# Performance work log

Measured on AMD Instinct MI355X. Metric: run time of the kernel, lower is better.

Reference implementation:

```python
import jax, jax.numpy as jnp
import numpy as np

EMBED_SIZE = 1024
HEADS = 16
HEAD_DIM = EMBED_SIZE // HEADS


def setup_inputs() -> dict:
    key = jax.random.key(0)
    k1, k2, k3, k4 = jax.random.split(key, 4)
    N, L = 4, 2048
    return {
        "values": jax.random.normal(k1, (N, L, EMBED_SIZE), dtype=jnp.float32),
        "keys": jax.random.normal(k2, (N, L, EMBED_SIZE), dtype=jnp.float32),
        "query": jax.random.normal(k3, (N, L, EMBED_SIZE), dtype=jnp.float32),
        "w_out": jax.random.normal(k4, (EMBED_SIZE, EMBED_SIZE), dtype=jnp.float32) * (1.0 / np.sqrt(EMBED_SIZE)),
        "b_out": jnp.zeros((EMBED_SIZE,), dtype=jnp.float32),
    }


def reference(values, keys, query, w_out, b_out):
    N, q_len, _ = query.shape
    v_len = values.shape[1]
    k_len = keys.shape[1]
    # split heads: (N, L, H, D). NOTE: source never applies the per-head
    # q/k/v Linear layers in forward, so raw inputs are used directly.
    v = values.reshape(N, v_len, HEADS, HEAD_DIM)
    k = keys.reshape(N, k_len, HEADS, HEAD_DIM)
    q = query.reshape(N, q_len, HEADS, HEAD_DIM)
    # energy: (N, H, Q, K); scale by sqrt(embed_size) as in the source
    energy = jnp.einsum('nqhd,nkhd->nhqk', q, k)
    attn = jax.nn.softmax(energy / jnp.sqrt(jnp.float32(EMBED_SIZE)), axis=3)
    out = jnp.einsum('nhql,nlhd->nqhd', attn, v).reshape(N, q_len, EMBED_SIZE)
    # fc_out: x @ W.T + b (torch Linear convention)
    return out @ w_out.T + b_out
```

## Files before the change

### kernel.cpp

```cpp
#include <hip/hip_runtime.h>
#include <hip/hip_bf16.h>

#define NB 4
#define LSEQ 2048
#define NH 16
#define HD 64
#define EMB 1024

typedef __attribute__((ext_vector_type(8))) short bf16x8;
typedef __attribute__((ext_vector_type(4))) float f32x4;
typedef __attribute__((ext_vector_type(16))) float f32x16;
typedef __attribute__((ext_vector_type(2))) unsigned int uint2v;

__device__ __forceinline__ unsigned short f2bf(float x) {
    union { float f; unsigned u; } v; v.f = x;
    unsigned r = v.u + 0x7fff + ((v.u >> 16) & 1);
    return (unsigned short)(r >> 16);
}

__device__ __forceinline__ float exp2_fast(float x) {
#if __has_builtin(__builtin_amdgcn_exp2f)
    return __builtin_amdgcn_exp2f(x);
#else
    float r; asm("v_exp_f32 %0, %1\n\ts_nop 1" : "=v"(r) : "v"(x)); return r;
#endif
}

__device__ __forceinline__ unsigned pack_bf2(float lo, float hi) {
    union { __hip_bfloat162 h2; unsigned u; } cv;
    cv.h2 = __float22bfloat162_rn(make_float2(lo, hi));
    return cv.u;
}

__device__ __forceinline__ void plswap(unsigned &a, unsigned &b) {
#if __has_builtin(__builtin_amdgcn_permlane32_swap)
    uint2v r = __builtin_amdgcn_permlane32_swap(a, b, false, false);
    a = r[0]; b = r[1];
#else
    asm volatile("s_nop 0\n\tv_permlane32_swap_b32 %0, %1\n\ts_nop 0"
                 : "+v"(a), "+v"(b));
#endif
}

__device__ __forceinline__ void async16(void* lds, const void* g) {
    __builtin_amdgcn_global_load_lds(
        (const __attribute__((address_space(1))) unsigned int*)g,
        (__attribute__((address_space(3))) unsigned int*)lds, 16, 0, 0);
}

__global__ void wconv_kernel(const float* __restrict__ Wf, unsigned short* __restrict__ Wb) {
    int i = (blockIdx.x * 256 + threadIdx.x) * 4;
    float4 v = *(const float4*)(Wf + i);
    ushort4 o = { f2bf(v.x), f2bf(v.y), f2bf(v.z), f2bf(v.w) };
    *(ushort4*)(Wb + i) = o;
}

__global__ void prep_all(const float* __restrict__ Wf, unsigned short* __restrict__ Wb,
                         const float* __restrict__ Kf, unsigned short* __restrict__ Kb,
                         const float* __restrict__ Vf, unsigned short* __restrict__ Vt)
{
    __shared__ float T[64][65];
    const int tid = threadIdx.x;
    const int b = blockIdx.x;

    if (b < 1024) {
        int i = (b * 256 + tid) * 4;
        float4 v = *(const float4*)(Wf + i);
        ushort4 o = { f2bf(v.x), f2bf(v.y), f2bf(v.z), f2bf(v.w) };
        *(ushort4*)(Wb + i) = o;
        return;
    }
    if (b < 5120) {
        int idx = (b - 1024) * 256 + tid;
        int c   = idx & 7;
        int key = (idx >> 3) & 2047;
        int h   = (idx >> 14) & 15;
        int n   = idx >> 18;
        const float* src = Kf + (size_t)(n * LSEQ + key) * EMB + h * HD + c * 8;
        float4 a = *(const float4*)src;
        float4 bb = *(const float4*)(src + 4);
        unsigned short* dst = Kb + (((size_t)(n * NH + h) * LSEQ + key) << 6)
                                 + ((c ^ (key & 7)) << 3);
        ushort4 o0 = { f2bf(a.x), f2bf(a.y), f2bf(a.z), f2bf(a.w) };
        ushort4 o1 = { f2bf(bb.x), f2bf(bb.y), f2bf(bb.z), f2bf(bb.w) };
        *(ushort4*)dst = o0;
        *(ushort4*)(dst + 4) = o1;
        return;
    }
    {
        const int vb = b - 5120;
        const int kt = vb & 31, h = (vb >> 5) & 15, n = vb >> 9;
        const float* src = Vf + (size_t)(n * LSEQ + kt * 64) * EMB + h * HD;
        unsigned short* dst = Vt + ((size_t)vb << 12);

        for (int i = tid; i < 1024; i += 256) {
            const int key = i >> 4;
            const int c4  = (i & 15) * 4;
            const float4 v = *(const float4*)(src + (size_t)key * EMB + c4);
            T[key][c4 + 0] = v.x; T[key][c4 + 1] = v.y;
            T[key][c4 + 2] = v.z; T[key][c4 + 3] = v.w;
        }
        __syncthreads();
        for (int i = tid; i < 512; i += 256) {
            const int d = i >> 3, c = i & 7;
            ushort4 o0 = { f2bf(T[c * 8 + 0][d]), f2bf(T[c * 8 + 1][d]),
                           f2bf(T[c * 8 + 2][d]), f2bf(T[c * 8 + 3][d]) };
            ushort4 o1 = { f2bf(T[c * 8 + 4][d]), f2bf(T[c * 8 + 5][d]),
                           f2bf(T[c * 8 + 6][d]), f2bf(T[c * 8 + 7][d]) };
            unsigned short* p = dst + (d << 6) + ((c ^ (d & 7)) << 3);
            *(ushort4*)p = o0;
            *(ushort4*)(p + 4) = o1;
        }
    }
}

__global__ __launch_bounds__(256, 2)
void attn13_kernel(const float* __restrict__ Qq, const unsigned short* __restrict__ Kb,
                   const unsigned short* __restrict__ Vt, unsigned short* __restrict__ X)
{
    __shared__ unsigned short Kl[3][4096];
    __shared__ unsigned short Vl[3][4096];

    const int tid  = threadIdx.x;
    const int lane = tid & 63;
    const int w    = tid >> 6;
    const int l31  = lane & 31;
    const int hl   = lane >> 5;
    const int swz7 = lane & 7;
    const int l    = ((blockIdx.x & 7) << 6) + (blockIdx.x >> 3);
    const int nh   = l >> 3;
    const int qtile = l & 7;
    const int n = nh >> 4, h = nh & 15;
    const int qrow0 = qtile * 256 + w * 64;

    bf16x8 ones;
    #pragma unroll
    for (int e = 0; e < 8; ++e) ones[e] = (short)0x3F80;

    const float qscale = 0.03125f * 1.44269504f;
    bf16x8 qf[2][4];
    #pragma unroll
    for (int g = 0; g < 2; ++g) {
        const float* qp = Qq + (size_t)(n * LSEQ + qrow0 + g * 32 + l31) * EMB + h * HD + hl * 8;
        #pragma unroll
        for (int dk = 0; dk < 4; ++dk) {
            bf16x8 t;
            #pragma unroll
            for (int e = 0; e < 8; ++e) t[e] = (short)f2bf(qp[dk * 16 + e] * qscale);
            qf[g][dk] = t;
        }
    }

    f32x16 oaccT[2][2];
    f32x16 lacc[2];
    #pragma unroll
    for (int g = 0; g < 2; ++g) {
        #pragma unroll
        for (int e = 0; e < 16; ++e) lacc[g][e] = 0.f;
        #pragma unroll
        for (int db = 0; db < 2; ++db)
            #pragma unroll
            for (int e = 0; e < 16; ++e) oaccT[g][db][e] = 0.f;
    }

    const unsigned short* kg0 = Kb + ((size_t)nh << 17);
    const unsigned short* vg0 = Vt + ((size_t)nh << 17);
    const int t8 = tid << 3;

#define ATTN_STAGE(buf, kt)                                                  \
    {                                                                        \
        const unsigned short* kg = kg0 + ((kt) << 12) + t8;                  \
        const unsigned short* vg = vg0 + ((kt) << 12) + t8;                  \
        async16(&Kl[buf][t8],        kg);                                    \
        async16(&Kl[buf][t8 + 2048], kg + 2048);                             \
        async16(&Vl[buf][t8],        vg);                                    \
        async16(&Vl[buf][t8 + 2048], vg + 2048);                             \
    }

    ATTN_STAGE(0, 0)
    ATTN_STAGE(1, 1)
    asm volatile("s_waitcnt vmcnt(4)" ::: "memory");
    __builtin_amdgcn_s_barrier();

    int cur = 0;
    for (int kt = 0; kt < LSEQ / 64; ++kt) {
        if (kt + 2 < LSEQ / 64) {
            const int pre = cur >= 1 ? cur - 1 : cur + 2;
            ATTN_STAGE(pre, kt + 2)
        }

        #pragma unroll
        for (int kb = 0; kb < 2; ++kb) {
            f32x16 sk[2];
            #pragma unroll
            for (int g = 0; g < 2; ++g)
                #pragma unroll
                for (int e = 0; e < 16; ++e) sk[g][e] = 0.f;
            #pragma unroll
            for (int dk = 0; dk < 4; ++dk) {
                bf16x8 ka = *(const bf16x8*)&Kl[cur][((kb * 32 + l31) << 6) + (((2 * dk + hl) ^ swz7) << 3)];
                #pragma unroll
                for (int g = 0; g < 2; ++g)
                    sk[g] = __builtin_amdgcn_mfma_f32_32x32x16_bf16(ka, qf[g][dk], sk[g], 0, 0, 0);
            }

            unsigned wgt[2][4][2];
            #pragma unroll
            for (int g = 0; g < 2; ++g) {
                float p[16];
                #pragma unroll
                for (int e = 0; e < 16; ++e) p[e] = exp2_fast(sk[g][e]);
                #pragma unroll
                for (int gg = 0; gg < 4; ++gg) {
                    wgt[g][gg][0] = pack_bf2(p[4 * gg + 0], p[4 * gg + 1]);
                    wgt[g][gg][1] = pack_bf2(p[4 * gg + 2], p[4 * gg + 3]);
                }
                plswap(wgt[g][0][0], wgt[g][1][0]); plswap(wgt[g][0][1], wgt[g][1][1]);
                plswap(wgt[g][2][0], wgt[g][3][0]); plswap(wgt[g][2][1], wgt[g][3][1]);
            }

            #pragma unroll
            for (int ks = 0; ks < 2; ++ks) {
                union { unsigned u[4]; bf16x8 v; } pu[2];
                #pragma unroll
                for (int g = 0; g < 2; ++g) {
                    pu[g].u[0] = wgt[g][2 * ks + 0][0];
                    pu[g].u[1] = wgt[g][2 * ks + 0][1];
                    pu[g].u[2] = wgt[g][2 * ks + 1][0];
                    pu[g].u[3] = wgt[g][2 * ks + 1][1];
                    lacc[g] = __builtin_amdgcn_mfma_f32_32x32x16_bf16(ones, pu[g].v, lacc[g], 0, 0, 0);
                }
                #pragma unroll
                for (int db = 0; db < 2; ++db) {
                    bf16x8 va = *(const bf16x8*)&Vl[cur][((db * 32 + l31) << 6) + (((4 * kb + 2 * ks + hl) ^ swz7) << 3)];
                    #pragma unroll
                    for (int g = 0; g < 2; ++g)
                        oaccT[g][db] = __builtin_amdgcn_mfma_f32_32x32x16_bf16(va, pu[g].v, oaccT[g][db], 0, 0, 0);
                }
            }
        }

        if (kt + 2 < LSEQ / 64) {
            asm volatile("s_waitcnt vmcnt(4)" ::: "memory");
        } else {
            asm volatile("s_waitcnt vmcnt(0)" ::: "memory");
        }
        __builtin_amdgcn_s_barrier();
        cur = cur < 2 ? cur + 1 : 0;
    }

    #pragma unroll
    for (int g = 0; g < 2; ++g) {
        const float rcp = 1.0f / lacc[g][0];
        unsigned ow0[4][2], ow1[4][2];
        #pragma unroll
        for (int gg = 0; gg < 4; ++gg) {
            ow0[gg][0] = pack_bf2(oaccT[g][0][4 * gg + 0] * rcp, oaccT[g][0][4 * gg + 1] * rcp);
            ow0[gg][1] = pack_bf2(oaccT[g][0][4 * gg + 2] * rcp, oaccT[g][0][4 * gg + 3] * rcp);
            ow1[gg][0] = pack_bf2(oaccT[g][1][4 * gg + 0] * rcp, oaccT[g][1][4 * gg + 1] * rcp);
            ow1[gg][1] = pack_bf2(oaccT[g][1][4 * gg + 2] * rcp, oaccT[g][1][4 * gg + 3] * rcp);
        }
        #pragma unroll
        for (int gg = 0; gg < 4; ++gg) {
            plswap(ow0[gg][0], ow1[gg][0]);
            plswap(ow0[gg][1], ow1[gg][1]);
        }
        unsigned short* xrow = X + (size_t)(n * LSEQ + qrow0 + g * 32 + l31) * EMB + h * HD + hl * 32;
        #pragma unroll
        for (int gg = 0; gg < 4; ++gg) {
            uint4 st = { ow0[gg][0], ow0[gg][1], ow1[gg][0], ow1[gg][1] };
            *(uint4*)(xrow + 8 * gg) = st;
        }
    }
}

#define KPAD 72
#define PPAD 72

__global__ __launch_bounds__(256, 2)
void attn_kernel(const float* __restrict__ Vv, const float* __restrict__ Kk,
                 const float* __restrict__ Qq, unsigned short* __restrict__ X)
{
    __shared__ unsigned short Klds[64 * KPAD];
    __shared__ unsigned short Vtlds[64 * KPAD];
    __shared__ unsigned short Plds[4 * 16 * PPAD];

    const int tid  = threadIdx.x;
    const int lane = tid & 63;
    const int w    = tid >> 6;
    const int l15  = lane & 15;
    const int l4   = lane >> 4;
    const int qtile = blockIdx.x;
    const int nh    = blockIdx.y;
    const int n = nh >> 4, h = nh & 15;

    bf16x8 qf[2];
    {
        const int qrow = qtile * 64 + w * 16 + l15;
        const float* qp = Qq + (size_t)(n * LSEQ + qrow) * EMB + h * HD + l4 * 8;
        for (int kk = 0; kk < 2; ++kk) {
            bf16x8 t;
            #pragma unroll
            for (int e = 0; e < 8; ++e) t[e] = (short)f2bf(qp[kk * 32 + e] * 0.03125f);
            qf[kk] = t;
        }
    }

    f32x4 oacc[4];
    #pragma unroll
    for (int f = 0; f < 4; ++f) oacc[f] = (f32x4){0.f, 0.f, 0.f, 0.f};
    float mrun[4], lrun[4];
    #pragma unroll
    for (int r = 0; r < 4; ++r) { mrun[r] = -1e30f; lrun[r] = 0.f; }

    for (int kt = 0; kt < LSEQ / 64; ++kt) {
        __syncthreads();
        for (int i = tid; i < 1024; i += 256) {
            const int row = i >> 4;
            const int c4  = (i & 15) * 4;
            const size_t gb = (size_t)(n * LSEQ + kt * 64 + row) * EMB + h * HD + c4;
            const float4 kv = *(const float4*)(Kk + gb);
            const float4 vv = *(const float4*)(Vv + gb);
            ushort4 k4 = { f2bf(kv.x), f2bf(kv.y), f2bf(kv.z), f2bf(kv.w) };
            *(ushort4*)&Klds[row * KPAD + c4] = k4;
            Vtlds[(c4 + 0) * KPAD + row] = f2bf(vv.x);
            Vtlds[(c4 + 1) * KPAD + row] = f2bf(vv.y);
            Vtlds[(c4 + 2) * KPAD + row] = f2bf(vv.z);
            Vtlds[(c4 + 3) * KPAD + row] = f2bf(vv.w);
        }
        __syncthreads();

        f32x4 s[4];
        #pragma unroll
        for (int f = 0; f < 4; ++f) {
            f32x4 acc = (f32x4){0.f, 0.f, 0.f, 0.f};
            #pragma unroll
            for (int kk = 0; kk < 2; ++kk) {
                bf16x8 kb = *(const bf16x8*)&Klds[(f * 16 + l15) * KPAD + kk * 32 + l4 * 8];
                acc = __builtin_amdgcn_mfma_f32_16x16x32_bf16(qf[kk], kb, acc, 0, 0, 0);
            }
            s[f] = acc;
        }

        float mnew[4], corr[4];
        #pragma unroll
        for (int r = 0; r < 4; ++r) {
            float m0 = fmaxf(fmaxf(s[0][r], s[1][r]), fmaxf(s[2][r], s[3][r]));
            #pragma unroll
            for (int msk = 1; msk < 16; msk <<= 1) m0 = fmaxf(m0, __shfl_xor(m0, msk));
            mnew[r] = fmaxf(mrun[r], m0);
            corr[r] = __expf(mrun[r] - mnew[r]);
        }
        float psum[4] = {0.f, 0.f, 0.f, 0.f};
        #pragma unroll
        for (int f = 0; f < 4; ++f) {
            #pragma unroll
            for (int r = 0; r < 4; ++r) {
                float p = __expf(s[f][r] - mnew[r]);
                psum[r] += p;
                Plds[(w * 16 + l4 * 4 + r) * PPAD + f * 16 + l15] = f2bf(p);
            }
        }
        #pragma unroll
        for (int r = 0; r < 4; ++r) {
            float t = psum[r];
            #pragma unroll
            for (int msk = 1; msk < 16; msk <<= 1) t += __shfl_xor(t, msk);
            lrun[r] = lrun[r] * corr[r] + t;
            mrun[r] = mnew[r];
        }
        #pragma unroll
        for (int f = 0; f < 4; ++f) {
            #pragma unroll
            for (int r = 0; r < 4; ++r) oacc[f][r] *= corr[r];
        }
        __syncthreads();

        #pragma unroll
        for (int ks = 0; ks < 2; ++ks) {
            bf16x8 pa = *(const bf16x8*)&Plds[(w * 16 + l15) * PPAD + ks * 32 + l4 * 8];
            #pragma unroll
            for (int f = 0; f < 4; ++f) {
                bf16x8 vb = *(const bf16x8*)&Vtlds[(f * 16 + l15) * KPAD + ks * 32 + l4 * 8];
                oacc[f] = __builtin_amdgcn_mfma_f32_16x16x32_bf16(pa, vb, oacc[f], 0, 0, 0);
            }
        }
    }

    #pragma unroll
    for (int f = 0; f < 4; ++f) {
        #pragma unroll
        for (int r = 0; r < 4; ++r) {
            const int qrow = qtile * 64 + w * 16 + l4 * 4 + r;
            const float o = oacc[f][r] / lrun[r];
            X[(size_t)(n * LSEQ + qrow) * EMB + h * HD + f * 16 + l15] = f2bf(o);
        }
    }
}

__global__ __launch_bounds__(256, 2)
void proj4_kernel(const unsigned short* __restrict__ X, const unsigned short* __restrict__ Wb,
                  const float* __restrict__ bias, float* __restrict__ out)
{
    __shared__ unsigned short Al[2][8192];
    __shared__ unsigned short Bl[2][8192];

    const int tid  = threadIdx.x;
    const int lane = tid & 63;
    const int w    = tid >> 6;
    const int l15  = lane & 15;
    const int l4   = lane >> 4;
    const int bid  = blockIdx.x;
    const int bm   = (bid & 7) * 8 + ((bid >> 3) & 7);
    const int bn   = bid >> 6;
    const int wr = (w >> 1) * 64;
    const int wc = (w & 1) * 64;

    f32x4 acc[4][4];
    #pragma unroll
    for (int i = 0; i < 4; ++i)
        #pragma unroll
        for (int j = 0; j < 4; ++j) acc[i][j] = (f32x4){0.f, 0.f, 0.f, 0.f};

    int srow[4], soff[4];
    #pragma unroll
    for (int j = 0; j < 4; ++j) {
        const int cid = tid + j * 256;
        srow[j] = cid >> 3;
        const int c = cid & 7;
        soff[j] = ((c ^ (srow[j] & 7)) << 3);
    }

#define PROJ_STAGE(buf, k0)                                                          \
    {                                                                                \
        _Pragma("unroll")                                                            \
        for (int j = 0; j < 4; ++j) {                                                \
            const int cid = tid + j * 256;                                           \
            async16(&Al[buf][cid << 3],                                              \
                    &X [(size_t)(bm * 128 + srow[j]) * EMB + (k0) + soff[j]]);       \
            async16(&Bl[buf][cid << 3],                                              \
                    &Wb[(size_t)(bn * 128 + srow[j]) * EMB + (k0) + soff[j]]);       \
        }                                                                            \
    }

    PROJ_STAGE(0, 0)
    asm volatile("s_waitcnt vmcnt(0)" ::: "memory");
    __syncthreads();

    int cur = 0;
    for (int k0 = 0; k0 < EMB; k0 += 64) {
        if (k0 + 64 < EMB) PROJ_STAGE(cur ^ 1, k0 + 64)

        #pragma unroll
        for (int kk = 0; kk < 2; ++kk) {
            bf16x8 af[4], bfr[4];
            #pragma unroll
            for (int i = 0; i < 4; ++i) {
                const int row = wr + i * 16 + l15;
                af[i] = *(const bf16x8*)&Al[cur][(row << 6) + (((kk * 4 + l4) ^ (row & 7)) << 3)];
            }
            #pragma unroll
            for (int j = 0; j < 4; ++j) {
                const int row = wc + j * 16 + l15;
                bfr[j] = *(const bf16x8*)&Bl[cur][(row << 6) + (((kk * 4 + l4) ^ (row & 7)) << 3)];
            }
            #pragma unroll
            for (int i = 0; i < 4; ++i)
                #pragma unroll
                for (int j = 0; j < 4; ++j)
                    acc[i][j] = __builtin_amdgcn_mfma_f32_16x16x32_bf16(af[i], bfr[j], acc[i][j], 0, 0, 0);
        }

        asm volatile("s_waitcnt vmcnt(0)" ::: "memory");
        __syncthreads();
        cur ^= 1;
    }

    #pragma unroll
    for (int i = 0; i < 4; ++i) {
        const int row = bm * 128 + wr + i * 16 + l4 * 4;
        #pragma unroll
        for (int j = 0; j < 4; ++j) {
            const int col = bn * 128 + wc + j * 16 + l15;
            const float bj = bias[col];
            #pragma unroll
            for (int r = 0; r < 4; ++r)
                out[(size_t)(row + r) * EMB + col] = acc[i][j][r] + bj;
        }
    }
}

extern "C" void kernel_launch(void* const* d_in, const int* in_sizes, int n_in,
                              void* d_out, int out_size, void* d_ws, size_t ws_size,
                              hipStream_t stream) {
    const float* Vv   = (const float*)d_in[0];
    const float* Kk   = (const float*)d_in[1];
    const float* Qq   = (const float*)d_in[2];
    const float* Wf   = (const float*)d_in[3];
    const float* bias = (const float*)d_in[4];
    float* out = (float*)d_out;

    unsigned short* X  = (unsigned short*)d_ws;
    unsigned short* Wb = (unsigned short*)((char*)d_ws + (size_t)16 * 1024 * 1024);
    const size_t need = (size_t)50 * 1024 * 1024;

    if (ws_size >= need) {
        unsigned short* Kb = (unsigned short*)((char*)d_ws + (size_t)18 * 1024 * 1024);
        unsigned short* Vt = (unsigned short*)((char*)d_ws + (size_t)34 * 1024 * 1024);
        prep_all<<<dim3(7168), 256, 0, stream>>>(Wf, Wb, Kk, Kb, Vv, Vt);
        attn13_kernel<<<dim3(512), 256, 0, stream>>>(Qq, Kb, Vt, X);
    } else {
        wconv_kernel<<<dim3(EMB * EMB / 1024), 256, 0, stream>>>(Wf, Wb);
        attn_kernel<<<dim3(LSEQ / 64, NB * NH), 256, 0, stream>>>(Vv, Kk, Qq, X);
    }

    proj4_kernel<<<dim3(512), 256, 0, stream>>>(X, Wb, bias, out);
}
```

Measured before the change: 128.0 us.

## Load K/V fragments directly from global into registers, drop LDS staging

The prep kernel now writes K and V in an MFMA-fragment-ready layout in 32-key chunks, so the attention kernel can load operand fragments straight from global memory into registers. This removes the LDS triple buffer, the async copies and the per-tile barriers, using a two-deep register double buffer for K instead. The row-sum is computed with scalar adds plus a cross-half shuffle rather than an extra MFMA against a ones vector. The cost is that global/L2 latency is now exposed per wave, with less prefetch depth, and each wave reloads K/V separately instead of sharing them through LDS.

Result: no change. 125.5 us (-1.9%).

```diff
diff --git a/kernel.cpp b/kernel.cpp
--- a/kernel.cpp
+++ b/kernel.cpp
@@ -79,8 +79,8 @@
         const float* src = Kf + (size_t)(n * LSEQ + key) * EMB + h * HD + c * 8;
         float4 a = *(const float4*)src;
         float4 bb = *(const float4*)(src + 4);
-        unsigned short* dst = Kb + (((size_t)(n * NH + h) * LSEQ + key) << 6)
-                                 + ((c ^ (key & 7)) << 3);
+        unsigned short* dst = Kb + ((size_t)((n * NH + h) * 64 + (key >> 5)) << 11)
+                                 + (((c << 5) + (key & 31)) << 3);
         ushort4 o0 = { f2bf(a.x), f2bf(a.y), f2bf(a.z), f2bf(a.w) };
         ushort4 o1 = { f2bf(bb.x), f2bf(bb.y), f2bf(bb.z), f2bf(bb.w) };
         *(ushort4*)dst = o0;
@@ -91,7 +91,7 @@
         const int vb = b - 5120;
         const int kt = vb & 31, h = (vb >> 5) & 15, n = vb >> 9;
         const float* src = Vf + (size_t)(n * LSEQ + kt * 64) * EMB + h * HD;
-        unsigned short* dst = Vt + ((size_t)vb << 12);
+        (void)n; (void)h; (void)kt;
 
         for (int i = tid; i < 1024; i += 256) {
             const int key = i >> 4;
@@ -102,41 +102,99 @@
         }
         __syncthreads();
         for (int i = tid; i < 512; i += 256) {
-            const int d = i >> 3, c = i & 7;
-            ushort4 o0 = { f2bf(T[c * 8 + 0][d]), f2bf(T[c * 8 + 1][d]),
-                           f2bf(T[c * 8 + 2][d]), f2bf(T[c * 8 + 3][d]) };
-            ushort4 o1 = { f2bf(T[c * 8 + 4][d]), f2bf(T[c * 8 + 5][d]),
-                           f2bf(T[c * 8 + 6][d]), f2bf(T[c * 8 + 7][d]) };
-            unsigned short* p = dst + (d << 6) + ((c ^ (d & 7)) << 3);
+            const int d = i >> 3, half = (i >> 2) & 1, c2 = i & 3;
+            const int k0 = half * 32 + c2 * 8;
+            ushort4 o0 = { f2bf(T[k0 + 0][d]), f2bf(T[k0 + 1][d]),
+                           f2bf(T[k0 + 2][d]), f2bf(T[k0 + 3][d]) };
+            ushort4 o1 = { f2bf(T[k0 + 4][d]), f2bf(T[k0 + 5][d]),
+                           f2bf(T[k0 + 6][d]), f2bf(T[k0 + 7][d]) };
+            unsigned short* p = Vt + ((size_t)(vb * 2 + half) << 11)
+                                   + (((c2 << 6) + d) << 3);
             *(ushort4*)p = o0;
             *(ushort4*)(p + 4) = o1;
         }
     }
 }
 
+
+__device__ __forceinline__ void attn14_body(
+    const bf16x8 (&KF)[4], const unsigned short* __restrict__ vb_,
+    const bf16x8 (&qf)[2][4], const int hl, const int l31,
+    f32x16 (&oaccT)[2][2], float (&lp)[2])
+{
+    bf16x8 vf[4];
+    #pragma unroll
+    for (int i = 0; i < 4; ++i) {
+        const int ks = i >> 1, db = i & 1;
+        vf[i] = *(const bf16x8*)(vb_ + ((((ks << 1) + hl) << 6) + (db << 5) + l31) * 8);
+    }
+
+    f32x16 sk[2];
+    #pragma unroll
+    for (int g = 0; g < 2; ++g)
+        #pragma unroll
+        for (int e = 0; e < 16; ++e) sk[g][e] = 0.f;
+    #pragma unroll
+    for (int dk = 0; dk < 4; ++dk)
+        #pragma unroll
+        for (int g = 0; g < 2; ++g)
+            sk[g] = __builtin_amdgcn_mfma_f32_32x32x16_bf16(KF[dk], qf[g][dk], sk[g], 0, 0, 0);
+
+    unsigned wgt[2][4][2];
+    #pragma unroll
+    for (int g = 0; g < 2; ++g) {
+        float p[16];
+        #pragma unroll
+        for (int e = 0; e < 16; ++e) p[e] = exp2_fast(sk[g][e]);
+        {
+            float t0 = (p[0] + p[1]) + (p[2] + p[3]);
+            float t1 = (p[4] + p[5]) + (p[6] + p[7]);
+            float t2 = (p[8] + p[9]) + (p[10] + p[11]);
+            float t3 = (p[12] + p[13]) + (p[14] + p[15]);
+            lp[g] += (t0 + t1) + (t2 + t3);
+        }
+        #pragma unroll
+        for (int gg = 0; gg < 4; ++gg) {
+            wgt[g][gg][0] = pack_bf2(p[4 * gg + 0], p[4 * gg + 1]);
+            wgt[g][gg][1] = pack_bf2(p[4 * gg + 2], p[4 * gg + 3]);
+        }
+        plswap(wgt[g][0][0], wgt[g][1][0]); plswap(wgt[g][0][1], wgt[g][1][1]);
+        plswap(wgt[g][2][0], wgt[g][3][0]); plswap(wgt[g][2][1], wgt[g][3][1]);
+    }
+
+    #pragma unroll
+    for (int ks = 0; ks < 2; ++ks) {
+        union { unsigned u[4]; bf16x8 v; } pu[2];
+        #pragma unroll
+        for (int g = 0; g < 2; ++g) {
+            pu[g].u[0] = wgt[g][2 * ks + 0][0];
+            pu[g].u[1] = wgt[g][2 * ks + 0][1];
+            pu[g].u[2] = wgt[g][2 * ks + 1][0];
+            pu[g].u[3] = wgt[g][2 * ks + 1][1];
+        }
+        #pragma unroll
+        for (int db = 0; db < 2; ++db)
+            #pragma unroll
+            for (int g = 0; g < 2; ++g)
+                oaccT[g][db] = __builtin_amdgcn_mfma_f32_32x32x16_bf16(vf[ks * 2 + db], pu[g].v, oaccT[g][db], 0, 0, 0);
+    }
+}
+
 __global__ __launch_bounds__(256, 2)
-void attn13_kernel(const float* __restrict__ Qq, const unsigned short* __restrict__ Kb,
+void attn14_kernel(const float* __restrict__ Qq, const unsigned short* __restrict__ Kb,
                    const unsigned short* __restrict__ Vt, unsigned short* __restrict__ X)
 {
-    __shared__ unsigned short Kl[3][4096];
-    __shared__ unsigned short Vl[3][4096];
-
     const int tid  = threadIdx.x;
     const int lane = tid & 63;
     const int w    = tid >> 6;
     const int l31  = lane & 31;
     const int hl   = lane >> 5;
-    const int swz7 = lane & 7;
     const int l    = ((blockIdx.x & 7) << 6) + (blockIdx.x >> 3);
     const int nh   = l >> 3;
     const int qtile = l & 7;
     const int n = nh >> 4, h = nh & 15;
     const int qrow0 = qtile * 256 + w * 64;
 
-    bf16x8 ones;
-    #pragma unroll
-    for (int e = 0; e < 8; ++e) ones[e] = (short)0x3F80;
-
     const float qscale = 0.03125f * 1.44269504f;
     bf16x8 qf[2][4];
     #pragma unroll
@@ -152,106 +210,37 @@
     }
 
     f32x16 oaccT[2][2];
-    f32x16 lacc[2];
-    #pragma unroll
-    for (int g = 0; g < 2; ++g) {
-        #pragma unroll
-        for (int e = 0; e < 16; ++e) lacc[g][e] = 0.f;
+    float lp[2] = {0.f, 0.f};
+    #pragma unroll
+    for (int g = 0; g < 2; ++g)
         #pragma unroll
         for (int db = 0; db < 2; ++db)
             #pragma unroll
             for (int e = 0; e < 16; ++e) oaccT[g][db][e] = 0.f;
-    }
 
     const unsigned short* kg0 = Kb + ((size_t)nh << 17);
     const unsigned short* vg0 = Vt + ((size_t)nh << 17);
-    const int t8 = tid << 3;
-
-#define ATTN_STAGE(buf, kt)                                                  \
-    {                                                                        \
-        const unsigned short* kg = kg0 + ((kt) << 12) + t8;                  \
-        const unsigned short* vg = vg0 + ((kt) << 12) + t8;                  \
-        async16(&Kl[buf][t8],        kg);                                    \
-        async16(&Kl[buf][t8 + 2048], kg + 2048);                             \
-        async16(&Vl[buf][t8],        vg);                                    \
-        async16(&Vl[buf][t8 + 2048], vg + 2048);                             \
-    }
-
-    ATTN_STAGE(0, 0)
-    ATTN_STAGE(1, 1)
-    asm volatile("s_waitcnt vmcnt(4)" ::: "memory");
-    __builtin_amdgcn_s_barrier();
-
-    int cur = 0;
-    for (int kt = 0; kt < LSEQ / 64; ++kt) {
-        if (kt + 2 < LSEQ / 64) {
-            const int pre = cur >= 1 ? cur - 1 : cur + 2;
-            ATTN_STAGE(pre, kt + 2)
-        }
-
-        #pragma unroll
-        for (int kb = 0; kb < 2; ++kb) {
-            f32x16 sk[2];
-            #pragma unroll
-            for (int g = 0; g < 2; ++g)
-                #pragma unroll
-                for (int e = 0; e < 16; ++e) sk[g][e] = 0.f;
-            #pragma unroll
-            for (int dk = 0; dk < 4; ++dk) {
-                bf16x8 ka = *(const bf16x8*)&Kl[cur][((kb * 32 + l31) << 6) + (((2 * dk + hl) ^ swz7) << 3)];
-                #pragma unroll
-                for (int g = 0; g < 2; ++g)
-                    sk[g] = __builtin_amdgcn_mfma_f32_32x32x16_bf16(ka, qf[g][dk], sk[g], 0, 0, 0);
-            }
-
-            unsigned wgt[2][4][2];
-            #pragma unroll
-            for (int g = 0; g < 2; ++g) {
-                float p[16];
-                #pragma unroll
-                for (int e = 0; e < 16; ++e) p[e] = exp2_fast(sk[g][e]);
-                #pragma unroll
-                for (int gg = 0; gg < 4; ++gg) {
-                    wgt[g][gg][0] = pack_bf2(p[4 * gg + 0], p[4 * gg + 1]);
-                    wgt[g][gg][1] = pack_bf2(p[4 * gg + 2], p[4 * gg + 3]);
-                }
-                plswap(wgt[g][0][0], wgt[g][1][0]); plswap(wgt[g][0][1], wgt[g][1][1]);
-                plswap(wgt[g][2][0], wgt[g][3][0]); plswap(wgt[g][2][1], wgt[g][3][1]);
-            }
-
-            #pragma unroll
-            for (int ks = 0; ks < 2; ++ks) {
-                union { unsigned u[4]; bf16x8 v; } pu[2];
-                #pragma unroll
-                for (int g = 0; g < 2; ++g) {
-                    pu[g].u[0] = wgt[g][2 * ks + 0][0];
-                    pu[g].u[1] = wgt[g][2 * ks + 0][1];
-                    pu[g].u[2] = wgt[g][2 * ks + 1][0];
-                    pu[g].u[3] = wgt[g][2 * ks + 1][1];
-                    lacc[g] = __builtin_amdgcn_mfma_f32_32x32x16_bf16(ones, pu[g].v, lacc[g], 0, 0, 0);
-                }
-                #pragma unroll
-                for (int db = 0; db < 2; ++db) {
-                    bf16x8 va = *(const bf16x8*)&Vl[cur][((db * 32 + l31) << 6) + (((4 * kb + 2 * ks + hl) ^ swz7) << 3)];
-                    #pragma unroll
-                    for (int g = 0; g < 2; ++g)
-                        oaccT[g][db] = __builtin_amdgcn_mfma_f32_32x32x16_bf16(va, pu[g].v, oaccT[g][db], 0, 0, 0);
-                }
-            }
-        }
-
-        if (kt + 2 < LSEQ / 64) {
-            asm volatile("s_waitcnt vmcnt(4)" ::: "memory");
-        } else {
-            asm volatile("s_waitcnt vmcnt(0)" ::: "memory");
-        }
-        __builtin_amdgcn_s_barrier();
-        cur = cur < 2 ? cur + 1 : 0;
+
+    bf16x8 kA[4], kB[4];
+    auto LOADK = [&](bf16x8 (&KF)[4], int tau) {
+        const unsigned short* kb_ = kg0 + ((size_t)tau << 11);
+        #pragma unroll
+        for (int dk = 0; dk < 4; ++dk)
+            KF[dk] = *(const bf16x8*)(kb_ + ((((dk << 1) + hl) << 5) + l31) * 8);
+    };
+
+    LOADK(kA, 0);
+    for (int tt = 0; tt < 32; ++tt) {
+        LOADK(kB, 2 * tt + 1);
+        attn14_body(kA, vg0 + ((size_t)(2 * tt) << 11), qf, hl, l31, oaccT, lp);
+        if (tt < 31) LOADK(kA, 2 * tt + 2);
+        attn14_body(kB, vg0 + ((size_t)(2 * tt + 1) << 11), qf, hl, l31, oaccT, lp);
     }
 
     #pragma unroll
     for (int g = 0; g < 2; ++g) {
-        const float rcp = 1.0f / lacc[g][0];
+        const float ltot = lp[g] + __shfl_xor(lp[g], 32);
+        const float rcp = 1.0f / ltot;
         unsigned ow0[4][2], ow1[4][2];
         #pragma unroll
         for (int gg = 0; gg < 4; ++gg) {
@@ -508,7 +497,7 @@
         unsigned short* Kb = (unsigned short*)((char*)d_ws + (size_t)18 * 1024 * 1024);
         unsigned short* Vt = (unsigned short*)((char*)d_ws + (size_t)34 * 1024 * 1024);
         prep_all<<<dim3(7168), 256, 0, stream>>>(Wf, Wb, Kk, Kb, Vv, Vt);
-        attn13_kernel<<<dim3(512), 256, 0, stream>>>(Qq, Kb, Vt, X);
+        attn14_kernel<<<dim3(512), 256, 0, stream>>>(Qq, Kb, Vt, X);
     } else {
         wconv_kernel<<<dim3(EMB * EMB / 1024), 256, 0, stream>>>(Wf, Wb);
         attn_kernel<<<dim3(LSEQ / 64, NB * NH), 256, 0, stream>>>(Vv, Kk, Qq, X);
```
